# Kernel tuning notes

Hardware: AMD Instinct MI355X
Metric: run time of the kernel (lower is better)

The kernel has to match this reference:

```python
import jax, jax.numpy as jnp
import numpy as np

N_NODES = 100000
HIDDEN = 64
N_EDGES = 1600000


def _sage_conv(x, edge_index, Wl, Wr, b):
    # PyG SAGEConv (mean aggr): out_i = W_l @ mean_{j->i} x_j + W_r @ x_i + b
    src, dst = edge_index[0], edge_index[1]
    msg = x[src]                                      # [E, H] gather
    agg = jax.ops.segment_sum(msg, dst, num_segments=N_NODES)  # [N, H]
    deg = jax.ops.segment_sum(jnp.ones((msg.shape[0],), x.dtype), dst,
                              num_segments=N_NODES)
    agg = agg / jnp.maximum(deg, 1.0)[:, None]
    return agg @ Wl.T + x @ Wr.T + b


def setup_inputs() -> dict:
    key = jax.random.key(0)
    ks = jax.random.split(key, 8)
    s = 1.0 / np.sqrt(HIDDEN)
    return {
        "emb": jax.random.normal(ks[0], (N_NODES, HIDDEN), jnp.float32),
        "Wl1": jax.random.normal(ks[1], (HIDDEN, HIDDEN), jnp.float32) * s,
        "Wr1": jax.random.normal(ks[2], (HIDDEN, HIDDEN), jnp.float32) * s,
        "b1": jnp.zeros((HIDDEN,), jnp.float32),
        "Wl2": jax.random.normal(ks[3], (HIDDEN, HIDDEN), jnp.float32) * s,
        "Wr2": jax.random.normal(ks[4], (HIDDEN, HIDDEN), jnp.float32) * s,
        "b2": jnp.zeros((HIDDEN,), jnp.float32),
        "node_id": jnp.arange(N_NODES, dtype=jnp.int64 if jax.config.jax_enable_x64 else jnp.int32),
        "edge_index": jax.random.randint(ks[5], (2, N_EDGES), 0, N_NODES),
    }


def reference(emb, Wl1, Wr1, b1, Wl2, Wr2, b2, node_id, edge_index):
    # Embedding lookup
    x = emb[node_id]                                   # [N, H]
    # GNN: relu(conv1) -> conv2
    x = jax.nn.relu(_sage_conv(x, edge_index, Wl1, Wr1, b1))
    x = _sage_conv(x, edge_index, Wl2, Wr2, b2)
    # Classifier: per-edge dot product of endpoint features
    ef1 = x[edge_index[0]]                             # [E, H]
    ef2 = x[edge_index[1]]                             # [E, H]
    return (ef1 * ef2).sum(axis=-1)                    # [E]
```

## Files before the change

kernel.cpp:

```cpp
#include <hip/hip_runtime.h>

#define N_NODES 100000
#define HID 64
#define N_EDGES 1600000
#define NB 391
#define C_EPB 6400

typedef __attribute__((ext_vector_type(8))) short bf16x8;
typedef __attribute__((ext_vector_type(4))) float f32x4;

__device__ __forceinline__ unsigned short f2bf(float f) {
    unsigned u = __float_as_uint(f);
    u = (u + 0x7FFFu + ((u >> 16) & 1u)) >> 16;
    return (unsigned short)u;
}
__device__ __forceinline__ float bf2f(unsigned short h) {
    return __uint_as_float(((unsigned)h) << 16);
}
__device__ __forceinline__ float bflo(unsigned w) { return __uint_as_float(w << 16); }
__device__ __forceinline__ float bfhi(unsigned w) { return __uint_as_float(w & 0xFFFF0000u); }

__global__ void gather_bf16_kernel(const float* __restrict__ emb,
                                   const int* __restrict__ nid,
                                   unsigned short* __restrict__ xh) {
    int i = blockIdx.x * blockDim.x + threadIdx.x;
    const int total = N_NODES * (HID / 4);
    if (i >= total) return;
    int row = i >> 4;
    int c   = i & 15;
    int s   = nid[row];
    float4 v = reinterpret_cast<const float4*>(emb)[(size_t)s * 16 + c];
    uint2 p;
    p.x = (unsigned)f2bf(v.x) | ((unsigned)f2bf(v.y) << 16);
    p.y = (unsigned)f2bf(v.z) | ((unsigned)f2bf(v.w) << 16);
    reinterpret_cast<uint2*>(xh)[(size_t)row * 16 + c] = p;
}

__global__ void bucket_hist(const int* __restrict__ dst,
                            int* __restrict__ bhist) {
    __shared__ int h[NB];
    for (int i = threadIdx.x; i < NB; i += blockDim.x) h[i] = 0;
    __syncthreads();
    int nt = gridDim.x * blockDim.x;
    const int4* d4 = (const int4*)dst;
    for (int q = blockIdx.x * blockDim.x + threadIdx.x; q < N_EDGES / 4; q += nt) {
        int4 v = d4[q];
        atomicAdd(&h[v.x >> 8], 1);
        atomicAdd(&h[v.y >> 8], 1);
        atomicAdd(&h[v.z >> 8], 1);
        atomicAdd(&h[v.w >> 8], 1);
    }
    __syncthreads();
    for (int i = threadIdx.x; i < NB; i += blockDim.x)
        if (h[i]) atomicAdd(&bhist[i], h[i]);
}

__global__ void bucket_scan(const int* __restrict__ bhist,
                            int* __restrict__ boff,
                            int* __restrict__ bcursor) {
    __shared__ int s[512];
    int v = (threadIdx.x < NB) ? bhist[threadIdx.x] : 0;
    s[threadIdx.x] = v;
    __syncthreads();
    for (int off = 1; off < 512; off <<= 1) {
        int t = (threadIdx.x >= off) ? s[threadIdx.x - off] : 0;
        __syncthreads();
        s[threadIdx.x] += t;
        __syncthreads();
    }
    if (threadIdx.x < NB) {
        int ex = s[threadIdx.x] - v;
        boff[threadIdx.x] = ex;
        bcursor[threadIdx.x] = ex;
    }
}

__global__ void bucket_scatter(const int* __restrict__ src,
                               const int* __restrict__ dst,
                               int* __restrict__ bcursor,
                               int2* __restrict__ pairs) {
    __shared__ int h[NB];
    __shared__ int base[NB];
    for (int i = threadIdx.x; i < NB; i += blockDim.x) h[i] = 0;
    __syncthreads();
    int e0 = blockIdx.x * C_EPB;
    int e1 = e0 + C_EPB; if (e1 > N_EDGES) e1 = N_EDGES;
    for (int e = e0 + threadIdx.x; e < e1; e += blockDim.x)
        atomicAdd(&h[dst[e] >> 8], 1);
    __syncthreads();
    for (int i = threadIdx.x; i < NB; i += blockDim.x) {
        int c = h[i];
        base[i] = c ? atomicAdd(&bcursor[i], c) : 0;
    }
    __syncthreads();
    for (int i = threadIdx.x; i < NB; i += blockDim.x) h[i] = 0;
    __syncthreads();
    for (int e = e0 + threadIdx.x; e < e1; e += blockDim.x) {
        int d = dst[e];
        int b = d >> 8;
        int slot = base[b] + atomicAdd(&h[b], 1);
        pairs[slot] = make_int2(src[e], d);
    }
}

__global__ void bucket_csr(const int2* __restrict__ pairs,
                           const int* __restrict__ boff,
                           const int* __restrict__ bcursor,
                           int* __restrict__ row_start,
                           int* __restrict__ adj) {
    __shared__ int cnt[256];
    __shared__ int sc[256];
    int b = blockIdx.x;
    int node0 = b << 8;
    int p0 = boff[b];
    int p1 = bcursor[b];
    int t = threadIdx.x;
    cnt[t] = 0;
    __syncthreads();
    for (int p = p0 + t; p < p1; p += 256)
        atomicAdd(&cnt[pairs[p].y & 255], 1);
    __syncthreads();
    int v = cnt[t];
    sc[t] = v;
    __syncthreads();
    for (int off = 1; off < 256; off <<= 1) {
        int u = (t >= off) ? sc[t - off] : 0;
        __syncthreads();
        sc[t] += u;
        __syncthreads();
    }
    sc[t] = p0 + sc[t] - v;
    __syncthreads();
    int node = node0 + t;
    if (node <= N_NODES) row_start[node] = sc[t];
    __syncthreads();
    for (int p = p0 + t; p < p1; p += 256) {
        int2 pr = pairs[p];
        int slot = atomicAdd(&sc[pr.y & 255], 1);
        adj[slot] = pr.x;
    }
}

__global__ void agg_kernel(const int* __restrict__ row_start,
                           const int* __restrict__ adj,
                           const unsigned short* __restrict__ xh,
                           unsigned short* __restrict__ M) {
    int lane = threadIdx.x & 63;
    int slot = lane >> 4;
    int c    = lane & 15;
    int wpb = blockDim.x >> 6;
    int wid = blockIdx.x * wpb + (threadIdx.x >> 6);
    int stride = gridDim.x * wpb;
    const uint2* xw = (const uint2*)xh;
    uint2* Mw = (uint2*)M;
    for (int row = wid; row < N_NODES; row += stride) {
        int beg = row_start[row], end = row_start[row + 1];
        float a0 = 0.f, a1 = 0.f, a2 = 0.f, a3 = 0.f;
        int j = beg + slot;
        for (; j + 12 < end; j += 16) {
            int s0 = adj[j], s1 = adj[j + 4], s2 = adj[j + 8], s3 = adj[j + 12];
            uint2 v0 = xw[(size_t)s0 * 16 + c];
            uint2 v1 = xw[(size_t)s1 * 16 + c];
            uint2 v2 = xw[(size_t)s2 * 16 + c];
            uint2 v3 = xw[(size_t)s3 * 16 + c];
            a0 += bflo(v0.x) + bflo(v1.x) + bflo(v2.x) + bflo(v3.x);
            a1 += bfhi(v0.x) + bfhi(v1.x) + bfhi(v2.x) + bfhi(v3.x);
            a2 += bflo(v0.y) + bflo(v1.y) + bflo(v2.y) + bflo(v3.y);
            a3 += bfhi(v0.y) + bfhi(v1.y) + bfhi(v2.y) + bfhi(v3.y);
        }
        for (; j < end; j += 4) {
            uint2 v = xw[(size_t)adj[j] * 16 + c];
            a0 += bflo(v.x); a1 += bfhi(v.x);
            a2 += bflo(v.y); a3 += bfhi(v.y);
        }
        a0 += __shfl_xor(a0, 16); a0 += __shfl_xor(a0, 32);
        a1 += __shfl_xor(a1, 16); a1 += __shfl_xor(a1, 32);
        a2 += __shfl_xor(a2, 16); a2 += __shfl_xor(a2, 32);
        a3 += __shfl_xor(a3, 16); a3 += __shfl_xor(a3, 32);
        if (slot == 0) {
            float inv = 1.0f / fmaxf((float)(end - beg), 1.0f);
            uint2 p;
            p.x = (unsigned)f2bf(a0 * inv) | ((unsigned)f2bf(a1 * inv) << 16);
            p.y = (unsigned)f2bf(a2 * inv) | ((unsigned)f2bf(a3 * inv) << 16);
            Mw[(size_t)row * 16 + c] = p;
        }
    }
}

__global__ void gemm_kernel(const unsigned short* __restrict__ Am,
                            const unsigned short* __restrict__ As,
                            const float* __restrict__ Wl,
                            const float* __restrict__ Wr,
                            const float* __restrict__ bias,
                            unsigned short* __restrict__ H,
                            int relu) {
    int lane = threadIdx.x & 63;
    int m = lane & 15, quad = lane >> 4;

    bf16x8 wf[2][2][4];
    for (int mat = 0; mat < 2; ++mat) {
        const float* W = mat ? Wr : Wl;
        for (int ks = 0; ks < 2; ++ks)
            for (int ct = 0; ct < 4; ++ct) {
                const float* p = W + (ct * 16 + m) * HID + ks * 32 + quad * 8;
                bf16x8 f;
                #pragma unroll
                for (int j = 0; j < 8; ++j) f[j] = (short)f2bf(p[j]);
                wf[mat][ks][ct] = f;
            }
    }
    float bv[4];
    #pragma unroll
    for (int ct = 0; ct < 4; ++ct) bv[ct] = bias[ct * 16 + m];

    int wpb = blockDim.x >> 6;
    int wid = blockIdx.x * wpb + (threadIdx.x >> 6);
    int stride = gridDim.x * wpb;
    const int NT = N_NODES / 16;
    for (int t = wid; t < NT; t += stride) {
        f32x4 acc[4] = {{0,0,0,0},{0,0,0,0},{0,0,0,0},{0,0,0,0}};
        size_t rowbase = ((size_t)t * 16 + m) * HID;
        #pragma unroll
        for (int ks = 0; ks < 2; ++ks) {
            bf16x8 a0 = *(const bf16x8*)(Am + rowbase + ks * 32 + quad * 8);
            bf16x8 a1 = *(const bf16x8*)(As + rowbase + ks * 32 + quad * 8);
            #pragma unroll
            for (int ct = 0; ct < 4; ++ct) {
                acc[ct] = __builtin_amdgcn_mfma_f32_16x16x32_bf16(a0, wf[0][ks][ct], acc[ct], 0, 0, 0);
                acc[ct] = __builtin_amdgcn_mfma_f32_16x16x32_bf16(a1, wf[1][ks][ct], acc[ct], 0, 0, 0);
            }
        }
        #pragma unroll
        for (int ct = 0; ct < 4; ++ct) {
            #pragma unroll
            for (int r = 0; r < 4; ++r) {
                float v = acc[ct][r] + bv[ct];
                if (relu) v = fmaxf(v, 0.f);
                H[((size_t)t * 16 + quad * 4 + r) * HID + ct * 16 + m] = f2bf(v);
            }
        }
    }
}

__global__ void edge_dot_kernel(const int* __restrict__ src,
                                const int* __restrict__ dst,
                                const unsigned short* __restrict__ h,
                                float* __restrict__ out) {
    int t = blockIdx.x * blockDim.x + threadIdx.x;
    int g = t >> 3;
    int c = t & 7;
    int e0 = g * 2;
    if (e0 >= N_EDGES) return;
    int a0 = src[e0],     b0 = dst[e0];
    int a1 = src[e0 + 1], b1 = dst[e0 + 1];
    const uint4* h4 = reinterpret_cast<const uint4*>(h);
    uint4 va0 = h4[(size_t)a0 * 8 + c];
    uint4 vb0 = h4[(size_t)b0 * 8 + c];
    uint4 va1 = h4[(size_t)a1 * 8 + c];
    uint4 vb1 = h4[(size_t)b1 * 8 + c];
    float p0 = bflo(va0.x) * bflo(vb0.x) + bfhi(va0.x) * bfhi(vb0.x)
             + bflo(va0.y) * bflo(vb0.y) + bfhi(va0.y) * bfhi(vb0.y)
             + bflo(va0.z) * bflo(vb0.z) + bfhi(va0.z) * bfhi(vb0.z)
             + bflo(va0.w) * bflo(vb0.w) + bfhi(va0.w) * bfhi(vb0.w);
    float p1 = bflo(va1.x) * bflo(vb1.x) + bfhi(va1.x) * bfhi(vb1.x)
             + bflo(va1.y) * bflo(vb1.y) + bfhi(va1.y) * bfhi(vb1.y)
             + bflo(va1.z) * bflo(vb1.z) + bfhi(va1.z) * bfhi(vb1.z)
             + bflo(va1.w) * bflo(vb1.w) + bfhi(va1.w) * bfhi(vb1.w);
    p0 += __shfl_xor(p0, 1); p0 += __shfl_xor(p0, 2); p0 += __shfl_xor(p0, 4);
    p1 += __shfl_xor(p1, 1); p1 += __shfl_xor(p1, 2); p1 += __shfl_xor(p1, 4);
    if (c == 0) reinterpret_cast<float2*>(out)[g] = make_float2(p0, p1);
}

extern "C" void kernel_launch(void* const* d_in, const int* in_sizes, int n_in,
                              void* d_out, int out_size, void* d_ws, size_t ws_size,
                              hipStream_t stream) {
    const float* emb = (const float*)d_in[0];
    const float* Wl1 = (const float*)d_in[1];
    const float* Wr1 = (const float*)d_in[2];
    const float* b1  = (const float*)d_in[3];
    const float* Wl2 = (const float*)d_in[4];
    const float* Wr2 = (const float*)d_in[5];
    const float* b2  = (const float*)d_in[6];
    const int*   nid = (const int*)d_in[7];
    const int*   ei  = (const int*)d_in[8];
    const int* esrc = ei;
    const int* edst = ei + N_EDGES;
    float* out = (float*)d_out;

    const size_t NH = (size_t)N_NODES * HID;
    unsigned short* xh  = (unsigned short*)d_ws;
    unsigned short* h1h = xh + NH;
    unsigned short* h2h = h1h + NH;
    unsigned short* M   = h2h + NH;
    int* ib        = (int*)(M + NH);
    int* row_start = ib;
    int* adj       = ib + N_NODES + 64;
    int2* pairs    = (int2*)(adj + N_EDGES + 64);
    int* bhist     = (int*)(pairs + N_EDGES);
    int* boff      = bhist + NB + 1;
    int* bcursor   = boff + NB + 1;

    hipMemsetAsync(bhist, 0, NB * sizeof(int), stream);

    gather_bf16_kernel<<<(N_NODES * 16 + 255) / 256, 256, 0, stream>>>(emb, nid, xh);

    bucket_hist<<<256, 256, 0, stream>>>(edst, bhist);
    bucket_scan<<<1, 512, 0, stream>>>(bhist, boff, bcursor);
    bucket_scatter<<<(N_EDGES + C_EPB - 1) / C_EPB, 256, 0, stream>>>(esrc, edst, bcursor, pairs);
    bucket_csr<<<NB, 256, 0, stream>>>(pairs, boff, bcursor, row_start, adj);

    agg_kernel<<<2048, 256, 0, stream>>>(row_start, adj, xh, M);
    gemm_kernel<<<512, 256, 0, stream>>>(M, xh, Wl1, Wr1, b1, h1h, 1);

    agg_kernel<<<2048, 256, 0, stream>>>(row_start, adj, h1h, M);
    gemm_kernel<<<512, 256, 0, stream>>>(M, h1h, Wl2, Wr2, b2, h2h, 0);

    edge_dot_kernel<<<((size_t)(N_EDGES / 2) * 8 + 255) / 256, 256, 0, stream>>>(esrc, edst, h2h, out);
}
```

Before: 304.3 us.

## Fuse gather with histogram, pack edge pairs into one int, vectorize scatter

Merges the embedding gather/bf16 conversion and the destination histogram into one launch, with disjoint block ranges handling each task. Edge pairs are packed into a single 32-bit word (source shifted left by 8, low 8 bits of destination), which halves the scratch traffic of the bucketing pass. The scatter now reads src/dst as int4 vectors. The GEMM grid grows from 512 to 782 blocks. The packing relies on node ids fitting in 24 bits, and the scatter's int4 reads assume the edge count divides evenly into blocks.

```diff
diff --git a/kernel.cpp b/kernel.cpp
--- a/kernel.cpp
+++ b/kernel.cpp
@@ -5,6 +5,7 @@
 #define N_EDGES 1600000
 #define NB 391
 #define C_EPB 6400
+#define G_GATHER 6250
 
 typedef __attribute__((ext_vector_type(8))) short bf16x8;
 typedef __attribute__((ext_vector_type(4))) float f32x4;
@@ -14,45 +15,42 @@
     u = (u + 0x7FFFu + ((u >> 16) & 1u)) >> 16;
     return (unsigned short)u;
 }
-__device__ __forceinline__ float bf2f(unsigned short h) {
-    return __uint_as_float(((unsigned)h) << 16);
-}
 __device__ __forceinline__ float bflo(unsigned w) { return __uint_as_float(w << 16); }
 __device__ __forceinline__ float bfhi(unsigned w) { return __uint_as_float(w & 0xFFFF0000u); }
 
-__global__ void gather_bf16_kernel(const float* __restrict__ emb,
+__global__ void gather_hist_kernel(const float* __restrict__ emb,
                                    const int* __restrict__ nid,
-                                   unsigned short* __restrict__ xh) {
-    int i = blockIdx.x * blockDim.x + threadIdx.x;
-    const int total = N_NODES * (HID / 4);
-    if (i >= total) return;
-    int row = i >> 4;
-    int c   = i & 15;
-    int s   = nid[row];
-    float4 v = reinterpret_cast<const float4*>(emb)[(size_t)s * 16 + c];
-    uint2 p;
-    p.x = (unsigned)f2bf(v.x) | ((unsigned)f2bf(v.y) << 16);
-    p.y = (unsigned)f2bf(v.z) | ((unsigned)f2bf(v.w) << 16);
-    reinterpret_cast<uint2*>(xh)[(size_t)row * 16 + c] = p;
-}
-
-__global__ void bucket_hist(const int* __restrict__ dst,
-                            int* __restrict__ bhist) {
+                                   unsigned short* __restrict__ xh,
+                                   const int* __restrict__ dst,
+                                   int* __restrict__ bhist) {
     __shared__ int h[NB];
-    for (int i = threadIdx.x; i < NB; i += blockDim.x) h[i] = 0;
-    __syncthreads();
-    int nt = gridDim.x * blockDim.x;
-    const int4* d4 = (const int4*)dst;
-    for (int q = blockIdx.x * blockDim.x + threadIdx.x; q < N_EDGES / 4; q += nt) {
-        int4 v = d4[q];
-        atomicAdd(&h[v.x >> 8], 1);
-        atomicAdd(&h[v.y >> 8], 1);
-        atomicAdd(&h[v.z >> 8], 1);
-        atomicAdd(&h[v.w >> 8], 1);
-    }
-    __syncthreads();
-    for (int i = threadIdx.x; i < NB; i += blockDim.x)
-        if (h[i]) atomicAdd(&bhist[i], h[i]);
+    if (blockIdx.x < G_GATHER) {
+        int i = blockIdx.x * blockDim.x + threadIdx.x;
+        int row = i >> 4;
+        int c   = i & 15;
+        int s   = nid[row];
+        float4 v = reinterpret_cast<const float4*>(emb)[(size_t)s * 16 + c];
+        uint2 p;
+        p.x = (unsigned)f2bf(v.x) | ((unsigned)f2bf(v.y) << 16);
+        p.y = (unsigned)f2bf(v.z) | ((unsigned)f2bf(v.w) << 16);
+        reinterpret_cast<uint2*>(xh)[(size_t)row * 16 + c] = p;
+    } else {
+        int hb = blockIdx.x - G_GATHER;
+        for (int i = threadIdx.x; i < NB; i += blockDim.x) h[i] = 0;
+        __syncthreads();
+        int nt = 256 * blockDim.x;
+        const int4* d4 = (const int4*)dst;
+        for (int q = hb * blockDim.x + threadIdx.x; q < N_EDGES / 4; q += nt) {
+            int4 v = d4[q];
+            atomicAdd(&h[v.x >> 8], 1);
+            atomicAdd(&h[v.y >> 8], 1);
+            atomicAdd(&h[v.z >> 8], 1);
+            atomicAdd(&h[v.w >> 8], 1);
+        }
+        __syncthreads();
+        for (int i = threadIdx.x; i < NB; i += blockDim.x)
+            if (h[i]) atomicAdd(&bhist[i], h[i]);
+    }
 }
 
 __global__ void bucket_scan(const int* __restrict__ bhist,
@@ -78,15 +76,22 @@
 __global__ void bucket_scatter(const int* __restrict__ src,
                                const int* __restrict__ dst,
                                int* __restrict__ bcursor,
-                               int2* __restrict__ pairs) {
+                               int* __restrict__ pairs) {
     __shared__ int h[NB];
     __shared__ int base[NB];
     for (int i = threadIdx.x; i < NB; i += blockDim.x) h[i] = 0;
     __syncthreads();
-    int e0 = blockIdx.x * C_EPB;
-    int e1 = e0 + C_EPB; if (e1 > N_EDGES) e1 = N_EDGES;
-    for (int e = e0 + threadIdx.x; e < e1; e += blockDim.x)
-        atomicAdd(&h[dst[e] >> 8], 1);
+    int q0 = blockIdx.x * (C_EPB / 4);
+    int q1 = q0 + (C_EPB / 4);
+    const int4* d4 = (const int4*)dst;
+    const int4* s4 = (const int4*)src;
+    for (int q = q0 + threadIdx.x; q < q1; q += blockDim.x) {
+        int4 v = d4[q];
+        atomicAdd(&h[v.x >> 8], 1);
+        atomicAdd(&h[v.y >> 8], 1);
+        atomicAdd(&h[v.z >> 8], 1);
+        atomicAdd(&h[v.w >> 8], 1);
+    }
     __syncthreads();
     for (int i = threadIdx.x; i < NB; i += blockDim.x) {
         int c = h[i];
@@ -95,15 +100,18 @@
     __syncthreads();
     for (int i = threadIdx.x; i < NB; i += blockDim.x) h[i] = 0;
     __syncthreads();
-    for (int e = e0 + threadIdx.x; e < e1; e += blockDim.x) {
-        int d = dst[e];
-        int b = d >> 8;
-        int slot = base[b] + atomicAdd(&h[b], 1);
-        pairs[slot] = make_int2(src[e], d);
-    }
-}
-
-__global__ void bucket_csr(const int2* __restrict__ pairs,
+    for (int q = q0 + threadIdx.x; q < q1; q += blockDim.x) {
+        int4 d = d4[q];
+        int4 s = s4[q];
+        int b, slot;
+        b = d.x >> 8; slot = base[b] + atomicAdd(&h[b], 1); pairs[slot] = (s.x << 8) | (d.x & 255);
+        b = d.y >> 8; slot = base[b] + atomicAdd(&h[b], 1); pairs[slot] = (s.y << 8) | (d.y & 255);
+        b = d.z >> 8; slot = base[b] + atomicAdd(&h[b], 1); pairs[slot] = (s.z << 8) | (d.z & 255);
+        b = d.w >> 8; slot = base[b] + atomicAdd(&h[b], 1); pairs[slot] = (s.w << 8) | (d.w & 255);
+    }
+}
+
+__global__ void bucket_csr(const int* __restrict__ pairs,
                            const int* __restrict__ boff,
                            const int* __restrict__ bcursor,
                            int* __restrict__ row_start,
@@ -118,7 +126,7 @@
     cnt[t] = 0;
     __syncthreads();
     for (int p = p0 + t; p < p1; p += 256)
-        atomicAdd(&cnt[pairs[p].y & 255], 1);
+        atomicAdd(&cnt[pairs[p] & 255], 1);
     __syncthreads();
     int v = cnt[t];
     sc[t] = v;
@@ -135,9 +143,9 @@
     if (node <= N_NODES) row_start[node] = sc[t];
     __syncthreads();
     for (int p = p0 + t; p < p1; p += 256) {
-        int2 pr = pairs[p];
-        int slot = atomicAdd(&sc[pr.y & 255], 1);
-        adj[slot] = pr.x;
+        int pr = pairs[p];
+        int slot = atomicAdd(&sc[pr & 255], 1);
+        adj[slot] = ((unsigned)pr) >> 8;
     }
 }
 
@@ -295,25 +303,24 @@
     int* ib        = (int*)(M + NH);
     int* row_start = ib;
     int* adj       = ib + N_NODES + 64;
-    int2* pairs    = (int2*)(adj + N_EDGES + 64);
-    int* bhist     = (int*)(pairs + N_EDGES);
+    int* pairs     = adj + N_EDGES + 64;
+    int* bhist     = pairs + N_EDGES + 64;
     int* boff      = bhist + NB + 1;
     int* bcursor   = boff + NB + 1;
 
     hipMemsetAsync(bhist, 0, NB * sizeof(int), stream);
 
-    gather_bf16_kernel<<<(N_NODES * 16 + 255) / 256, 256, 0, stream>>>(emb, nid, xh);
-
-    bucket_hist<<<256, 256, 0, stream>>>(edst, bhist);
+    gather_hist_kernel<<<G_GATHER + 256, 256, 0, stream>>>(emb, nid, xh, edst, bhist);
+
     bucket_scan<<<1, 512, 0, stream>>>(bhist, boff, bcursor);
-    bucket_scatter<<<(N_EDGES + C_EPB - 1) / C_EPB, 256, 0, stream>>>(esrc, edst, bcursor, pairs);
+    bucket_scatter<<<N_EDGES / C_EPB, 256, 0, stream>>>(esrc, edst, bcursor, pairs);
     bucket_csr<<<NB, 256, 0, stream>>>(pairs, boff, bcursor, row_start, adj);
 
     agg_kernel<<<2048, 256, 0, stream>>>(row_start, adj, xh, M);
-    gemm_kernel<<<512, 256, 0, stream>>>(M, xh, Wl1, Wr1, b1, h1h, 1);
+    gemm_kernel<<<782, 256, 0, stream>>>(M, xh, Wl1, Wr1, b1, h1h, 1);
 
     agg_kernel<<<2048, 256, 0, stream>>>(row_start, adj, h1h, M);
-    gemm_kernel<<<512, 256, 0, stream>>>(M, h1h, Wl2, Wr2, b2, h2h, 0);
+    gemm_kernel<<<782, 256, 0, stream>>>(M, h1h, Wl2, Wr2, b2, h2h, 0);
 
     edge_dot_kernel<<<((size_t)(N_EDGES / 2) * 8 + 255) / 256, 256, 0, stream>>>(esrc, edst, h2h, out);
 }
```

New measurement: 305.0 us. About the same (+0.2%).
